# Performance work log

Measured on AMD Instinct MI355X. Metric: run time of the kernel, lower is better.

Reference implementation:

```python
import jax, jax.numpy as jnp
import numpy as np

B, NU, NT = 128, 32, 64          # batch, users/sample, antennas/sample
IN_F, H, OUT_F, NL = 128, 128, 16, 2
N_U, N_A = B * NU, B * NT        # total user / antenna nodes


def setup_inputs() -> dict:
    key = jax.random.key(0)
    ks = iter(jax.random.split(key, 40))
    p = lambda shape: jax.random.normal(next(ks), shape, jnp.float32) * 0.05
    inp = {
        'user_feat': jax.random.normal(next(ks), (N_U, IN_F), jnp.float32),
        'ant_noise': jax.random.normal(next(ks), (N_A, H), jnp.float32),
    }
    # complete bipartite edges within each batch sample
    b = np.arange(B)[:, None, None]
    u = np.arange(NU)[None, :, None]
    t = np.arange(NT)[None, None, :]
    su = np.broadcast_to(b * NU + u, (B, NU, NT)).reshape(-1)  # user global ids
    dt = np.broadcast_to(b * NT + t, (B, NU, NT)).reshape(-1)  # antenna global ids
    inp['src_u2a'] = jnp.asarray(su, jnp.int32)
    inp['dst_u2a'] = jnp.asarray(dt, jnp.int32)
    inp['src_a2u'] = jnp.asarray(dt, jnp.int32)
    inp['dst_a2u'] = jnp.asarray(su, jnp.int32)
    inp['W_ue'] = p((IN_F, H)); inp['b_ue'] = p((H,))
    inp['W_t'] = p((H, H));     inp['b_t'] = p((H,))
    for name in ['ca_aggr', 'ca_self', 'ca_comb', 'cu_aggr', 'cu_self', 'cu_comb']:
        inp[name + '_W'] = p((NL, H, H))
        inp[name + '_b'] = p((NL, H))
    inp['W_norm'] = p((H, OUT_F)); inp['b_norm'] = p((OUT_F,))
    return inp


def mlp(x, W, b):
    # stack of NL Linear(H,H) + ReLU, as in MLP module
    for i in range(W.shape[0]):
        x = jax.nn.relu(x @ W[i] + b[i])
    return x


def rel_conv(src_f, dst_f, src_idx, dst_idx, n_dst, aW, ab, sW, sb, cW, cb):
    # GraphConv2: mean-aggregate mlp_aggr(src) over in-edges, combine with mlp_self(dst)
    msg = mlp(src_f, aW, ab)                                   # [n_src, H]
    summed = jax.ops.segment_sum(msg[src_idx], dst_idx, num_segments=n_dst)
    deg = jax.ops.segment_sum(jnp.ones(dst_idx.shape, jnp.float32), dst_idx,
                              num_segments=n_dst)
    mean = summed / jnp.maximum(deg, 1.0)[:, None]
    return mlp(mlp(dst_f, sW, sb) + mean, cW, cb)


def reference(user_feat, ant_noise, src_u2a, dst_u2a, src_a2u, dst_a2u,
              W_ue, b_ue, W_t, b_t,
              ca_aggr_W, ca_aggr_b, ca_self_W, ca_self_b, ca_comb_W, ca_comb_b,
              cu_aggr_W, cu_aggr_b, cu_self_W, cu_self_b, cu_comb_W, cu_comb_b,
              W_norm, b_norm):
    # InitLayer
    hu = jax.nn.relu(user_feat @ W_ue + b_ue)                  # [B*NU, H]
    ant = jax.nn.relu(hu.reshape(B, NU, H).mean(axis=1) @ W_t + b_t)  # [B, H]
    ha = jnp.repeat(ant, NT, axis=0) + ant_noise               # [B*NT, H]
    # two applications of the SAME HeteroGraphConv (shared weights)
    for _ in range(2):
        na = rel_conv(hu, ha, src_u2a, dst_u2a, N_A,
                      ca_aggr_W, ca_aggr_b, ca_self_W, ca_self_b, ca_comb_W, ca_comb_b)
        nu = rel_conv(ha, hu, src_a2u, dst_a2u, N_U,
                      cu_aggr_W, cu_aggr_b, cu_self_W, cu_self_b, cu_comb_W, cu_comb_b)
        hu, ha = nu, na
    # NormLayer: project, split real/imag, normalize to unit modulus
    y = (ha @ W_norm + b_norm).reshape(B, NT, OUT_F)
    rf = OUT_F // 2
    re, im = y[..., :rf], y[..., rf:]
    mag = jnp.sqrt(re * re + im * im)
    return jnp.concatenate([re / mag, im / mag], axis=-1)      # [B, NT, OUT_F]
```

## Files before the change

### kernel.cpp

```cpp
#include <hip/hip_runtime.h>
#include <math.h>


using frag  = __attribute__((ext_vector_type(8))) short;
using f32x4 = __attribute__((ext_vector_type(4))) float;

#define LDST 136
#define SCOPE_AGT __HIP_MEMORY_SCOPE_AGENT

__device__ __forceinline__ float  bf2f(ushort u) { return __uint_as_float(((unsigned)u) << 16); }
__device__ __forceinline__ ushort f2bf(float f) {
    unsigned u = __float_as_uint(f);
    u += 0x7fff + ((u >> 16) & 1);
    return (ushort)(u >> 16);
}
__device__ __forceinline__ unsigned cvtpk(float lo, float hi) {
    unsigned r;
    asm("v_cvt_pk_bf16_f32 %0, %1, %2" : "=v"(r) : "v"(lo), "v"(hi));
    return r;
}
__device__ __forceinline__ void gst16_sc(void* p, f32x4 v) {
    asm volatile("global_store_dwordx4 %0, %1, off sc1" :: "v"(p), "v"(v) : "memory");
}

struct GP {
    const float *uf, *noise, *b_ue, *W_t, *b_t;
    const float *bias6[6];
    const float *Wn, *bn;
    const ushort *Wp;
    float *out;
    float *pE, *pA0, *pU0, *pA1;
    unsigned *flg;
};

struct PrepP { const float* Wm[13]; ushort* Wp; unsigned* flg; };

__global__ __launch_bounds__(512) void k_prep(PrepP Q)
{
    const int tid = threadIdx.x, blk = blockIdx.x;
    if (blk < 16) Q.flg[blk * 512 + tid] = 0;
    const int e = (blk * 512 + tid) * 8;
    const int l = (e >> 3) & 63, w = (e >> 9) & 7, kc = (e >> 12) & 3, m = e >> 14;
    const float* src = Q.Wm[m] + (kc * 32 + (l >> 4) * 8) * 128 + w * 16 + (l & 15);
    ushort h[8];
#pragma unroll
    for (int j = 0; j < 8; ++j) h[j] = f2bf(src[j * 128]);
    uint4 o = { (unsigned)h[0] | ((unsigned)h[1] << 16), (unsigned)h[2] | ((unsigned)h[3] << 16),
                (unsigned)h[4] | ((unsigned)h[5] << 16), (unsigned)h[6] | ((unsigned)h[7] << 16) };
    *(uint4*)(Q.Wp + e) = o;
}

__device__ __forceinline__ void psync(unsigned* myf, unsigned* pf, unsigned s) {
    asm volatile("s_waitcnt vmcnt(0)" ::: "memory");
    __syncthreads();
    if (threadIdx.x == 0) {
        __hip_atomic_store(myf, s, __ATOMIC_RELAXED, SCOPE_AGT);
        while (__hip_atomic_load(pf, __ATOMIC_RELAXED, SCOPE_AGT) < s)
            __builtin_amdgcn_s_sleep(1);
    }
    __syncthreads();
}

struct AF { frag f[4]; };
__device__ __forceinline__ AF ldA(const ushort* __restrict__ Wp, int mat, int tid)
{
    AF a;
    const ushort* base = Wp + ((size_t)mat << 14) + (tid << 3);
#pragma unroll
    for (int kc = 0; kc < 4; ++kc)
        a.f[kc] = *(const frag*)(base + (kc << 12));
    return a;
}

template<int MT, bool MEANADD, bool CS>
__device__ __forceinline__ void mlp_stage(const AF& A, const ushort* Xl, ushort* Yl,
    const float* biasL, const float* meanL, float* csL, float* __restrict__ csG,
    int n0, int l15, int q)
{
    const float4 bv = *(const float4*)(biasL + n0 + q * 4);
    float4 mv = {0.f, 0.f, 0.f, 0.f};
    if (MEANADD) mv = *(const float4*)(meanL + n0 + q * 4);
    float cs0 = 0.f, cs1 = 0.f, cs2 = 0.f, cs3 = 0.f;
#pragma unroll
    for (int mt = 0; mt < MT; ++mt) {
        frag Bv[4];
#pragma unroll
        for (int kc = 0; kc < 4; ++kc)
            Bv[kc] = *(const frag*)(Xl + (mt * 16 + l15) * LDST + kc * 32 + q * 8);
        f32x4 acc = {0.f, 0.f, 0.f, 0.f};
#pragma unroll
        for (int kc = 0; kc < 4; ++kc)
            acc = __builtin_amdgcn_mfma_f32_16x16x32_bf16(A.f[kc], Bv[kc], acc, 0, 0, 0);
        float v0 = acc[0] + bv.x, v1 = acc[1] + bv.y, v2 = acc[2] + bv.z, v3 = acc[3] + bv.w;
        v0 = v0 > 0.f ? v0 : 0.f; v1 = v1 > 0.f ? v1 : 0.f;
        v2 = v2 > 0.f ? v2 : 0.f; v3 = v3 > 0.f ? v3 : 0.f;
        if (MEANADD) { v0 += mv.x; v1 += mv.y; v2 += mv.z; v3 += mv.w; }
        if (CS) { cs0 += v0; cs1 += v1; cs2 += v2; cs3 += v3; }
        uint2 o = { cvtpk(v0, v1), cvtpk(v2, v3) };
        *(uint2*)(Yl + (mt * 16 + l15) * LDST + n0 + q * 4) = o;
    }
    if (CS) {
#pragma unroll
        for (int m = 1; m <= 8; m <<= 1) {
            cs0 += __shfl_xor(cs0, m); cs1 += __shfl_xor(cs1, m);
            cs2 += __shfl_xor(cs2, m); cs3 += __shfl_xor(cs3, m);
        }
        if (l15 == 0) {
            f32x4 t = { cs0, cs1, cs2, cs3 };
            *(f32x4*)(csL + n0 + q * 4) = t;
            gst16_sc(csG + n0 + q * 4, t);
        }
    }
}

__global__ __launch_bounds__(512, 1) void k_gnn(GP P)
{
    __shared__ __align__(16) ushort HU[16 * LDST];
    __shared__ __align__(16) ushort HA[32 * LDST];
    __shared__ __align__(16) ushort T0[32 * LDST];
    __shared__ __align__(16) ushort T1[32 * LDST];
    __shared__ __align__(16) float  biasL[1792];
    __shared__ __align__(16) float  redL[512];
    __shared__ __align__(16) float  meanP[128], meanQ[128], antL[128];

    const int blk = blockIdx.x, tid = threadIdx.x;
    const int b = blk & 127, half = blk >> 7, prt = blk ^ 128;
    const int lane = tid & 63, wave = tid >> 6;
    const int q = lane >> 4, l15 = lane & 15;
    const int n0 = wave * 16;
    unsigned* myf = P.flg + blk * 32;
    unsigned* prf = P.flg + prt * 32;

    AF An = ldA(P.Wp, 12, tid);

    {
        const int r = tid >> 5, k4 = tid & 31;
        const float4 v = *(const float4*)(P.uf + (size_t)(b * 32 + half * 16 + r) * 128 + k4 * 4);
        uint2 o = { cvtpk(v.x, v.y), cvtpk(v.z, v.w) };
        *(uint2*)(T0 + r * LDST + k4 * 4) = o;
    }
#pragma unroll
    for (int c = tid; c < 1024; c += 512) {
        const int r = c >> 5, k4 = c & 31;
        const float4 v = *(const float4*)(P.noise + (size_t)(b * 64 + half * 32 + r) * 128 + k4 * 4);
        uint2 o = { cvtpk(v.x, v.y), cvtpk(v.z, v.w) };
        *(uint2*)(HA + r * LDST + k4 * 4) = o;
    }
    if (tid < 128) biasL[tid] = P.b_ue[tid];
    if (tid < 128) biasL[1664 + tid] = P.b_t[tid];
#pragma unroll
    for (int r = 0; r < 6; ++r)
        if (tid < 256) biasL[128 + r * 256 + tid] = P.bias6[r][tid];
    __syncthreads();

    AF A;
    A = An; An = ldA(P.Wp, 0, tid);
    mlp_stage<1, false, true>(A, T0, HU, biasL + 0, nullptr, meanP, P.pE + blk * 128, n0, l15, q);
    __syncthreads();
    A = An; An = ldA(P.Wp, 1, tid);
    mlp_stage<1, false, false>(A, HU, T0, biasL + 128, nullptr, nullptr, nullptr, n0, l15, q);
    __syncthreads();
    A = An; An = ldA(P.Wp, 6, tid);
    mlp_stage<1, false, true>(A, T0, T1, biasL + 256, nullptr, meanQ, P.pA0 + blk * 128, n0, l15, q);
    __syncthreads();
    psync(myf, prf, 1u);

    if (tid < 128) {
        meanP[tid] = (meanP[tid] + P.pE[prt * 128 + tid]) * (1.f / 32.f);
        meanQ[tid] = (meanQ[tid] + P.pA0[prt * 128 + tid]) * (1.f / 32.f);
    }
    __syncthreads();
    {
        const int g = tid >> 7, col = tid & 127;
        float s = 0.f;
#pragma unroll 4
        for (int k = g * 32; k < g * 32 + 32; ++k) s += meanP[k] * P.W_t[k * 128 + col];
        redL[g * 128 + col] = s;
    }
    __syncthreads();
    if (tid < 128) {
        float a = biasL[1664 + tid] + redL[tid] + redL[128 + tid] + redL[256 + tid] + redL[384 + tid];
        antL[tid] = a > 0.f ? a : 0.f;
    }
    __syncthreads();
#pragma unroll
    for (int c = tid; c < 1024; c += 512) {
        const int r = c >> 5, k4 = c & 31;
        ushort4 h = *(ushort4*)(HA + r * LDST + k4 * 4);
        uint2 o = { cvtpk(bf2f(h.x) + antL[k4 * 4 + 0], bf2f(h.y) + antL[k4 * 4 + 1]),
                    cvtpk(bf2f(h.z) + antL[k4 * 4 + 2], bf2f(h.w) + antL[k4 * 4 + 3]) };
        *(uint2*)(HA + r * LDST + k4 * 4) = o;
    }
    __syncthreads();

    A = An; An = ldA(P.Wp, 7, tid);
    mlp_stage<2, false, false>(A, HA, T0, biasL + 896, nullptr, nullptr, nullptr, n0, l15, q);
    __syncthreads();
    A = An; An = ldA(P.Wp, 2, tid);
    mlp_stage<2, false, true>(A, T0, T1, biasL + 1024, nullptr, meanP, P.pU0 + blk * 128, n0, l15, q);
    __syncthreads();
    A = An; An = ldA(P.Wp, 3, tid);
    mlp_stage<2, false, false>(A, HA, T0, biasL + 384, nullptr, nullptr, nullptr, n0, l15, q);
    __syncthreads();
    psync(myf, prf, 2u);
    if (tid < 128)
        meanP[tid] = (meanP[tid] + P.pU0[prt * 128 + tid]) * (1.f / 64.f);
    __syncthreads();
    A = An; An = ldA(P.Wp, 4, tid);
    mlp_stage<2, true , false>(A, T0, T1, biasL + 512, meanQ, nullptr, nullptr, n0, l15, q);
    __syncthreads();
    A = An; An = ldA(P.Wp, 5, tid);
    mlp_stage<2, false, false>(A, T1, T0, biasL + 640, nullptr, nullptr, nullptr, n0, l15, q);
    __syncthreads();
    A = An; An = ldA(P.Wp, 8, tid);
    mlp_stage<2, false, false>(A, T0, HA, biasL + 768, nullptr, nullptr, nullptr, n0, l15, q);
    __syncthreads();
    A = An; An = ldA(P.Wp, 9, tid);
    mlp_stage<1, false, false>(A, HU, T0, biasL + 1152, nullptr, nullptr, nullptr, n0, l15, q);
    __syncthreads();
    A = An; An = ldA(P.Wp, 10, tid);
    mlp_stage<1, true , false>(A, T0, T1, biasL + 1280, meanP, nullptr, nullptr, n0, l15, q);
    __syncthreads();
    A = An; An = ldA(P.Wp, 11, tid);
    mlp_stage<1, false, false>(A, T1, T0, biasL + 1408, nullptr, nullptr, nullptr, n0, l15, q);
    __syncthreads();
    A = An; An = ldA(P.Wp, 0, tid);
    mlp_stage<1, false, false>(A, T0, HU, biasL + 1536, nullptr, nullptr, nullptr, n0, l15, q);
    __syncthreads();

    A = An; An = ldA(P.Wp, 1, tid);
    mlp_stage<1, false, false>(A, HU, T0, biasL + 128, nullptr, nullptr, nullptr, n0, l15, q);
    __syncthreads();
    A = An; An = ldA(P.Wp, 2, tid);
    mlp_stage<1, false, true>(A, T0, T1, biasL + 256, nullptr, meanQ, P.pA1 + blk * 128, n0, l15, q);
    __syncthreads();
    A = An; An = ldA(P.Wp, 3, tid);
    mlp_stage<2, false, false>(A, HA, T0, biasL + 384, nullptr, nullptr, nullptr, n0, l15, q);
    __syncthreads();
    psync(myf, prf, 3u);
    if (tid < 128)
        meanQ[tid] = (meanQ[tid] + P.pA1[prt * 128 + tid]) * (1.f / 32.f);
    __syncthreads();
    A = An; An = ldA(P.Wp, 4, tid);
    mlp_stage<2, true , false>(A, T0, T1, biasL + 512, meanQ, nullptr, nullptr, n0, l15, q);
    __syncthreads();
    A = An; An = ldA(P.Wp, 5, tid);
    mlp_stage<2, false, false>(A, T1, T0, biasL + 640, nullptr, nullptr, nullptr, n0, l15, q);
    __syncthreads();
    A = An;
    mlp_stage<2, false, false>(A, T0, T1, biasL + 768, nullptr, nullptr, nullptr, n0, l15, q);
    __syncthreads();

    float* WnS = (float*)T0;
    *(float4*)(WnS + tid * 4) = *(const float4*)(P.Wn + tid * 4);
    __syncthreads();
    {
        const int row = tid >> 4, j = tid & 15;
        float acc = P.bn[j];
        const ushort* h = T1 + row * LDST;
#pragma unroll 8
        for (int k = 0; k < 128; ++k) acc += bf2f(h[k]) * WnS[k * 16 + j];
        const float other = __shfl_xor(acc, 8);
        const float mag = sqrtf(acc * acc + other * other);
        P.out[(size_t)(b * 64 + half * 32 + row) * 16 + j] = acc / mag;
    }
}

extern "C" void kernel_launch(void* const* d_in, const int* in_sizes, int n_in,
                              void* d_out, int out_size, void* d_ws, size_t ws_size,
                              hipStream_t stream)
{
    GP P;
    P.uf    = (const float*)d_in[0];
    P.noise = (const float*)d_in[1];
    const float* W_ue = (const float*)d_in[6];
    P.b_ue  = (const float*)d_in[7];
    P.W_t   = (const float*)d_in[8];
    P.b_t   = (const float*)d_in[9];
    const float* caW[3] = {(const float*)d_in[10], (const float*)d_in[12], (const float*)d_in[14]};
    const float* cab[3] = {(const float*)d_in[11], (const float*)d_in[13], (const float*)d_in[15]};
    const float* cuW[3] = {(const float*)d_in[16], (const float*)d_in[18], (const float*)d_in[20]};
    const float* cub[3] = {(const float*)d_in[17], (const float*)d_in[19], (const float*)d_in[21]};
    P.Wn  = (const float*)d_in[22];
    P.bn  = (const float*)d_in[23];
    P.out = (float*)d_out;

    PrepP Q;
    Q.Wm[0]  = caW[0]; Q.Wm[1]  = caW[0] + 16384;
    Q.Wm[2]  = caW[1]; Q.Wm[3]  = caW[1] + 16384;
    Q.Wm[4]  = caW[2]; Q.Wm[5]  = caW[2] + 16384;
    Q.Wm[6]  = cuW[0]; Q.Wm[7]  = cuW[0] + 16384;
    Q.Wm[8]  = cuW[1]; Q.Wm[9]  = cuW[1] + 16384;
    Q.Wm[10] = cuW[2]; Q.Wm[11] = cuW[2] + 16384;
    Q.Wm[12] = W_ue;
    P.bias6[0] = cab[0]; P.bias6[1] = cab[1]; P.bias6[2] = cab[2];
    P.bias6[3] = cub[0]; P.bias6[4] = cub[1]; P.bias6[5] = cub[2];

    char* w = (char*)d_ws;
    P.flg = (unsigned*)w;
    P.pE  = (float*)(w + 32768);
    P.pA0 = P.pE  + 256 * 128;
    P.pU0 = P.pA0 + 256 * 128;
    P.pA1 = P.pU0 + 256 * 128;
    ushort* Wp = (ushort*)(w + 32768 + 4 * 256 * 128 * 4);
    Q.Wp = Wp;
    Q.flg = P.flg;
    P.Wp = Wp;

    k_prep<<<dim3(52), dim3(512), 0, stream>>>(Q);
    k_gnn<<<dim3(256), dim3(512), 0, stream>>>(P);
}
```

Measured before the change: 121.9 us.

## Merge per-sample block pairs into one 1024-thread block, dropping global flag syncs

Each batch sample is now handled by one 1024-thread block instead of two 512-thread blocks that exchanged partial column sums through global memory and spin-waited on flags. Rows are split across two wave groups, and column sums are combined in shared memory, which removes the cross-block atomics, sleeps and sc1 stores. The final projection loop now reads vectorised uint4 loads. In exchange only 128 blocks run on the GPU, each with twice the LDS footprint, so fewer CUs are occupied and each one has more per-block work.

```diff
diff --git a/kernel.cpp b/kernel.cpp
--- a/kernel.cpp
+++ b/kernel.cpp
@@ -6,7 +6,6 @@
 using f32x4 = __attribute__((ext_vector_type(4))) float;
 
 #define LDST 136
-#define SCOPE_AGT __HIP_MEMORY_SCOPE_AGENT
 
 __device__ __forceinline__ float  bf2f(ushort u) { return __uint_as_float(((unsigned)u) << 16); }
 __device__ __forceinline__ ushort f2bf(float f) {
@@ -18,9 +17,6 @@
     unsigned r;
     asm("v_cvt_pk_bf16_f32 %0, %1, %2" : "=v"(r) : "v"(lo), "v"(hi));
     return r;
-}
-__device__ __forceinline__ void gst16_sc(void* p, f32x4 v) {
-    asm volatile("global_store_dwordx4 %0, %1, off sc1" :: "v"(p), "v"(v) : "memory");
 }
 
 struct GP {
@@ -29,16 +25,13 @@
     const float *Wn, *bn;
     const ushort *Wp;
     float *out;
-    float *pE, *pA0, *pU0, *pA1;
-    unsigned *flg;
 };
 
-struct PrepP { const float* Wm[13]; ushort* Wp; unsigned* flg; };
+struct PrepP { const float* Wm[13]; ushort* Wp; };
 
 __global__ __launch_bounds__(512) void k_prep(PrepP Q)
 {
     const int tid = threadIdx.x, blk = blockIdx.x;
-    if (blk < 16) Q.flg[blk * 512 + tid] = 0;
     const int e = (blk * 512 + tid) * 8;
     const int l = (e >> 3) & 63, w = (e >> 9) & 7, kc = (e >> 12) & 3, m = e >> 14;
     const float* src = Q.Wm[m] + (kc * 32 + (l >> 4) * 8) * 128 + w * 16 + (l & 15);
@@ -50,22 +43,11 @@
     *(uint4*)(Q.Wp + e) = o;
 }
 
-__device__ __forceinline__ void psync(unsigned* myf, unsigned* pf, unsigned s) {
-    asm volatile("s_waitcnt vmcnt(0)" ::: "memory");
-    __syncthreads();
-    if (threadIdx.x == 0) {
-        __hip_atomic_store(myf, s, __ATOMIC_RELAXED, SCOPE_AGT);
-        while (__hip_atomic_load(pf, __ATOMIC_RELAXED, SCOPE_AGT) < s)
-            __builtin_amdgcn_s_sleep(1);
-    }
-    __syncthreads();
-}
-
 struct AF { frag f[4]; };
-__device__ __forceinline__ AF ldA(const ushort* __restrict__ Wp, int mat, int tid)
+__device__ __forceinline__ AF ldA(const ushort* __restrict__ Wp, int mat, int widx)
 {
     AF a;
-    const ushort* base = Wp + ((size_t)mat << 14) + (tid << 3);
+    const ushort* base = Wp + ((size_t)mat << 14) + (widx << 3);
 #pragma unroll
     for (int kc = 0; kc < 4; ++kc)
         a.f[kc] = *(const frag*)(base + (kc << 12));
@@ -74,8 +56,8 @@
 
 template<int MT, bool MEANADD, bool CS>
 __device__ __forceinline__ void mlp_stage(const AF& A, const ushort* Xl, ushort* Yl,
-    const float* biasL, const float* meanL, float* csL, float* __restrict__ csG,
-    int n0, int l15, int q)
+    const float* biasL, const float* meanL, float* csPart,
+    int row0, int n0, int l15, int q)
 {
     const float4 bv = *(const float4*)(biasL + n0 + q * 4);
     float4 mv = {0.f, 0.f, 0.f, 0.f};
@@ -83,10 +65,11 @@
     float cs0 = 0.f, cs1 = 0.f, cs2 = 0.f, cs3 = 0.f;
 #pragma unroll
     for (int mt = 0; mt < MT; ++mt) {
+        const int r = (row0 + mt * 16 + l15) * LDST;
         frag Bv[4];
 #pragma unroll
         for (int kc = 0; kc < 4; ++kc)
-            Bv[kc] = *(const frag*)(Xl + (mt * 16 + l15) * LDST + kc * 32 + q * 8);
+            Bv[kc] = *(const frag*)(Xl + r + kc * 32 + q * 8);
         f32x4 acc = {0.f, 0.f, 0.f, 0.f};
 #pragma unroll
         for (int kc = 0; kc < 4; ++kc)
@@ -97,7 +80,7 @@
         if (MEANADD) { v0 += mv.x; v1 += mv.y; v2 += mv.z; v3 += mv.w; }
         if (CS) { cs0 += v0; cs1 += v1; cs2 += v2; cs3 += v3; }
         uint2 o = { cvtpk(v0, v1), cvtpk(v2, v3) };
-        *(uint2*)(Yl + (mt * 16 + l15) * LDST + n0 + q * 4) = o;
+        *(uint2*)(Yl + r + n0 + q * 4) = o;
     }
     if (CS) {
 #pragma unroll
@@ -107,42 +90,42 @@
         }
         if (l15 == 0) {
             f32x4 t = { cs0, cs1, cs2, cs3 };
-            *(f32x4*)(csL + n0 + q * 4) = t;
-            gst16_sc(csG + n0 + q * 4, t);
+            *(f32x4*)(csPart + n0 + q * 4) = t;
         }
     }
 }
 
-__global__ __launch_bounds__(512, 1) void k_gnn(GP P)
-{
-    __shared__ __align__(16) ushort HU[16 * LDST];
-    __shared__ __align__(16) ushort HA[32 * LDST];
-    __shared__ __align__(16) ushort T0[32 * LDST];
-    __shared__ __align__(16) ushort T1[32 * LDST];
+__global__ __launch_bounds__(1024, 1) void k_gnn(GP P)
+{
+    __shared__ __align__(16) ushort HU[32 * LDST];
+    __shared__ __align__(16) ushort HA[64 * LDST];
+    __shared__ __align__(16) ushort T0[64 * LDST];
+    __shared__ __align__(16) ushort T1[64 * LDST];
     __shared__ __align__(16) float  biasL[1792];
-    __shared__ __align__(16) float  redL[512];
+    __shared__ __align__(16) float  redL[1024];
+    __shared__ __align__(16) float  csL[256];
     __shared__ __align__(16) float  meanP[128], meanQ[128], antL[128];
 
-    const int blk = blockIdx.x, tid = threadIdx.x;
-    const int b = blk & 127, half = blk >> 7, prt = blk ^ 128;
+    const int b = blockIdx.x, tid = threadIdx.x;
     const int lane = tid & 63, wave = tid >> 6;
+    const int wn = wave & 7, wm = wave >> 3;
     const int q = lane >> 4, l15 = lane & 15;
-    const int n0 = wave * 16;
-    unsigned* myf = P.flg + blk * 32;
-    unsigned* prf = P.flg + prt * 32;
-
-    AF An = ldA(P.Wp, 12, tid);
+    const int n0 = wn * 16, widx = wn * 64 + lane;
+    const int huR = wm * 16, haR = wm * 32;
+    float* csP = csL + wm * 128;
+
+    AF An = ldA(P.Wp, 12, widx);
 
     {
         const int r = tid >> 5, k4 = tid & 31;
-        const float4 v = *(const float4*)(P.uf + (size_t)(b * 32 + half * 16 + r) * 128 + k4 * 4);
+        const float4 v = *(const float4*)(P.uf + (size_t)(b * 32 + r) * 128 + k4 * 4);
         uint2 o = { cvtpk(v.x, v.y), cvtpk(v.z, v.w) };
         *(uint2*)(T0 + r * LDST + k4 * 4) = o;
     }
 #pragma unroll
-    for (int c = tid; c < 1024; c += 512) {
+    for (int c = tid; c < 2048; c += 1024) {
         const int r = c >> 5, k4 = c & 31;
-        const float4 v = *(const float4*)(P.noise + (size_t)(b * 64 + half * 32 + r) * 128 + k4 * 4);
+        const float4 v = *(const float4*)(P.noise + (size_t)(b * 64 + r) * 128 + k4 * 4);
         uint2 o = { cvtpk(v.x, v.y), cvtpk(v.z, v.w) };
         *(uint2*)(HA + r * LDST + k4 * 4) = o;
     }
@@ -154,37 +137,34 @@
     __syncthreads();
 
     AF A;
-    A = An; An = ldA(P.Wp, 0, tid);
-    mlp_stage<1, false, true>(A, T0, HU, biasL + 0, nullptr, meanP, P.pE + blk * 128, n0, l15, q);
-    __syncthreads();
-    A = An; An = ldA(P.Wp, 1, tid);
-    mlp_stage<1, false, false>(A, HU, T0, biasL + 128, nullptr, nullptr, nullptr, n0, l15, q);
-    __syncthreads();
-    A = An; An = ldA(P.Wp, 6, tid);
-    mlp_stage<1, false, true>(A, T0, T1, biasL + 256, nullptr, meanQ, P.pA0 + blk * 128, n0, l15, q);
-    __syncthreads();
-    psync(myf, prf, 1u);
-
-    if (tid < 128) {
-        meanP[tid] = (meanP[tid] + P.pE[prt * 128 + tid]) * (1.f / 32.f);
-        meanQ[tid] = (meanQ[tid] + P.pA0[prt * 128 + tid]) * (1.f / 32.f);
-    }
-    __syncthreads();
+    A = An; An = ldA(P.Wp, 0, widx);
+    mlp_stage<1, false, true>(A, T0, HU, biasL + 0, nullptr, csP, huR, n0, l15, q);
+    __syncthreads();
+    if (tid < 128) meanP[tid] = (csL[tid] + csL[128 + tid]) * (1.f / 32.f);
+    A = An; An = ldA(P.Wp, 1, widx);
+    mlp_stage<1, false, false>(A, HU, T0, biasL + 128, nullptr, nullptr, huR, n0, l15, q);
+    __syncthreads();
+    A = An; An = ldA(P.Wp, 6, widx);
+    mlp_stage<1, false, true>(A, T0, T1, biasL + 256, nullptr, csP, huR, n0, l15, q);
+    __syncthreads();
+    if (tid < 128) meanQ[tid] = (csL[tid] + csL[128 + tid]) * (1.f / 32.f);
     {
         const int g = tid >> 7, col = tid & 127;
         float s = 0.f;
 #pragma unroll 4
-        for (int k = g * 32; k < g * 32 + 32; ++k) s += meanP[k] * P.W_t[k * 128 + col];
+        for (int k = g * 16; k < g * 16 + 16; ++k) s += meanP[k] * P.W_t[k * 128 + col];
         redL[g * 128 + col] = s;
     }
     __syncthreads();
     if (tid < 128) {
-        float a = biasL[1664 + tid] + redL[tid] + redL[128 + tid] + redL[256 + tid] + redL[384 + tid];
+        float a = biasL[1664 + tid];
+#pragma unroll
+        for (int i = 0; i < 8; ++i) a += redL[i * 128 + tid];
         antL[tid] = a > 0.f ? a : 0.f;
     }
     __syncthreads();
 #pragma unroll
-    for (int c = tid; c < 1024; c += 512) {
+    for (int c = tid; c < 2048; c += 1024) {
         const int r = c >> 5, k4 = c & 31;
         ushort4 h = *(ushort4*)(HA + r * LDST + k4 * 4);
         uint2 o = { cvtpk(bf2f(h.x) + antL[k4 * 4 + 0], bf2f(h.y) + antL[k4 * 4 + 1]),
@@ -193,76 +173,77 @@
     }
     __syncthreads();
 
-    A = An; An = ldA(P.Wp, 7, tid);
-    mlp_stage<2, false, false>(A, HA, T0, biasL + 896, nullptr, nullptr, nullptr, n0, l15, q);
-    __syncthreads();
-    A = An; An = ldA(P.Wp, 2, tid);
-    mlp_stage<2, false, true>(A, T0, T1, biasL + 1024, nullptr, meanP, P.pU0 + blk * 128, n0, l15, q);
-    __syncthreads();
-    A = An; An = ldA(P.Wp, 3, tid);
-    mlp_stage<2, false, false>(A, HA, T0, biasL + 384, nullptr, nullptr, nullptr, n0, l15, q);
-    __syncthreads();
-    psync(myf, prf, 2u);
-    if (tid < 128)
-        meanP[tid] = (meanP[tid] + P.pU0[prt * 128 + tid]) * (1.f / 64.f);
-    __syncthreads();
-    A = An; An = ldA(P.Wp, 4, tid);
-    mlp_stage<2, true , false>(A, T0, T1, biasL + 512, meanQ, nullptr, nullptr, n0, l15, q);
-    __syncthreads();
-    A = An; An = ldA(P.Wp, 5, tid);
-    mlp_stage<2, false, false>(A, T1, T0, biasL + 640, nullptr, nullptr, nullptr, n0, l15, q);
-    __syncthreads();
-    A = An; An = ldA(P.Wp, 8, tid);
-    mlp_stage<2, false, false>(A, T0, HA, biasL + 768, nullptr, nullptr, nullptr, n0, l15, q);
-    __syncthreads();
-    A = An; An = ldA(P.Wp, 9, tid);
-    mlp_stage<1, false, false>(A, HU, T0, biasL + 1152, nullptr, nullptr, nullptr, n0, l15, q);
-    __syncthreads();
-    A = An; An = ldA(P.Wp, 10, tid);
-    mlp_stage<1, true , false>(A, T0, T1, biasL + 1280, meanP, nullptr, nullptr, n0, l15, q);
-    __syncthreads();
-    A = An; An = ldA(P.Wp, 11, tid);
-    mlp_stage<1, false, false>(A, T1, T0, biasL + 1408, nullptr, nullptr, nullptr, n0, l15, q);
-    __syncthreads();
-    A = An; An = ldA(P.Wp, 0, tid);
-    mlp_stage<1, false, false>(A, T0, HU, biasL + 1536, nullptr, nullptr, nullptr, n0, l15, q);
-    __syncthreads();
-
-    A = An; An = ldA(P.Wp, 1, tid);
-    mlp_stage<1, false, false>(A, HU, T0, biasL + 128, nullptr, nullptr, nullptr, n0, l15, q);
-    __syncthreads();
-    A = An; An = ldA(P.Wp, 2, tid);
-    mlp_stage<1, false, true>(A, T0, T1, biasL + 256, nullptr, meanQ, P.pA1 + blk * 128, n0, l15, q);
-    __syncthreads();
-    A = An; An = ldA(P.Wp, 3, tid);
-    mlp_stage<2, false, false>(A, HA, T0, biasL + 384, nullptr, nullptr, nullptr, n0, l15, q);
-    __syncthreads();
-    psync(myf, prf, 3u);
-    if (tid < 128)
-        meanQ[tid] = (meanQ[tid] + P.pA1[prt * 128 + tid]) * (1.f / 32.f);
-    __syncthreads();
-    A = An; An = ldA(P.Wp, 4, tid);
-    mlp_stage<2, true , false>(A, T0, T1, biasL + 512, meanQ, nullptr, nullptr, n0, l15, q);
-    __syncthreads();
-    A = An; An = ldA(P.Wp, 5, tid);
-    mlp_stage<2, false, false>(A, T1, T0, biasL + 640, nullptr, nullptr, nullptr, n0, l15, q);
+    A = An; An = ldA(P.Wp, 7, widx);
+    mlp_stage<2, false, false>(A, HA, T0, biasL + 896, nullptr, nullptr, haR, n0, l15, q);
+    __syncthreads();
+    A = An; An = ldA(P.Wp, 2, widx);
+    mlp_stage<2, false, true>(A, T0, T1, biasL + 1024, nullptr, csP, haR, n0, l15, q);
+    __syncthreads();
+    if (tid < 128) meanP[tid] = (csL[tid] + csL[128 + tid]) * (1.f / 64.f);
+    A = An; An = ldA(P.Wp, 3, widx);
+    mlp_stage<2, false, false>(A, HA, T0, biasL + 384, nullptr, nullptr, haR, n0, l15, q);
+    __syncthreads();
+    A = An; An = ldA(P.Wp, 4, widx);
+    mlp_stage<2, true , false>(A, T0, T1, biasL + 512, meanQ, nullptr, haR, n0, l15, q);
+    __syncthreads();
+    A = An; An = ldA(P.Wp, 5, widx);
+    mlp_stage<2, false, false>(A, T1, T0, biasL + 640, nullptr, nullptr, haR, n0, l15, q);
+    __syncthreads();
+    A = An; An = ldA(P.Wp, 8, widx);
+    mlp_stage<2, false, false>(A, T0, HA, biasL + 768, nullptr, nullptr, haR, n0, l15, q);
+    __syncthreads();
+    A = An; An = ldA(P.Wp, 9, widx);
+    mlp_stage<1, false, false>(A, HU, T0, biasL + 1152, nullptr, nullptr, huR, n0, l15, q);
+    __syncthreads();
+    A = An; An = ldA(P.Wp, 10, widx);
+    mlp_stage<1, true , false>(A, T0, T1, biasL + 1280, meanP, nullptr, huR, n0, l15, q);
+    __syncthreads();
+    A = An; An = ldA(P.Wp, 11, widx);
+    mlp_stage<1, false, false>(A, T1, T0, biasL + 1408, nullptr, nullptr, huR, n0, l15, q);
+    __syncthreads();
+    A = An; An = ldA(P.Wp, 0, widx);
+    mlp_stage<1, false, false>(A, T0, HU, biasL + 1536, nullptr, nullptr, huR, n0, l15, q);
+    __syncthreads();
+
+    A = An; An = ldA(P.Wp, 1, widx);
+    mlp_stage<1, false, false>(A, HU, T0, biasL + 128, nullptr, nullptr, huR, n0, l15, q);
+    __syncthreads();
+    A = An; An = ldA(P.Wp, 2, widx);
+    mlp_stage<1, false, true>(A, T0, T1, biasL + 256, nullptr, csP, huR, n0, l15, q);
+    __syncthreads();
+    if (tid < 128) meanQ[tid] = (csL[tid] + csL[128 + tid]) * (1.f / 32.f);
+    A = An; An = ldA(P.Wp, 3, widx);
+    mlp_stage<2, false, false>(A, HA, T0, biasL + 384, nullptr, nullptr, haR, n0, l15, q);
+    __syncthreads();
+    A = An; An = ldA(P.Wp, 4, widx);
+    mlp_stage<2, true , false>(A, T0, T1, biasL + 512, meanQ, nullptr, haR, n0, l15, q);
+    __syncthreads();
+    A = An; An = ldA(P.Wp, 5, widx);
+    mlp_stage<2, false, false>(A, T1, T0, biasL + 640, nullptr, nullptr, haR, n0, l15, q);
     __syncthreads();
     A = An;
-    mlp_stage<2, false, false>(A, T0, T1, biasL + 768, nullptr, nullptr, nullptr, n0, l15, q);
+    mlp_stage<2, false, false>(A, T0, T1, biasL + 768, nullptr, nullptr, haR, n0, l15, q);
     __syncthreads();
 
     float* WnS = (float*)T0;
-    *(float4*)(WnS + tid * 4) = *(const float4*)(P.Wn + tid * 4);
+    if (tid < 512) *(float4*)(WnS + tid * 4) = *(const float4*)(P.Wn + tid * 4);
     __syncthreads();
     {
         const int row = tid >> 4, j = tid & 15;
         float acc = P.bn[j];
-        const ushort* h = T1 + row * LDST;
-#pragma unroll 8
-        for (int k = 0; k < 128; ++k) acc += bf2f(h[k]) * WnS[k * 16 + j];
+        const uint4* h4 = (const uint4*)(T1 + row * LDST);
+#pragma unroll
+        for (int kb = 0; kb < 16; ++kb) {
+            const uint4 u = h4[kb];
+            const float* wp = WnS + kb * 128 + j;
+            acc += bf2f((ushort)u.x) * wp[0]   + bf2f((ushort)(u.x >> 16)) * wp[16]
+                 + bf2f((ushort)u.y) * wp[32]  + bf2f((ushort)(u.y >> 16)) * wp[48]
+                 + bf2f((ushort)u.z) * wp[64]  + bf2f((ushort)(u.z >> 16)) * wp[80]
+                 + bf2f((ushort)u.w) * wp[96]  + bf2f((ushort)(u.w >> 16)) * wp[112];
+        }
         const float other = __shfl_xor(acc, 8);
         const float mag = sqrtf(acc * acc + other * other);
-        P.out[(size_t)(b * 64 + half * 32 + row) * 16 + j] = acc / mag;
+        P.out[(size_t)(b * 64 + row) * 16 + j] = acc / mag;
     }
 }
 
@@ -296,17 +277,10 @@
     P.bias6[0] = cab[0]; P.bias6[1] = cab[1]; P.bias6[2] = cab[2];
     P.bias6[3] = cub[0]; P.bias6[4] = cub[1]; P.bias6[5] = cub[2];
 
-    char* w = (char*)d_ws;
-    P.flg = (unsigned*)w;
-    P.pE  = (float*)(w + 32768);
-    P.pA0 = P.pE  + 256 * 128;
-    P.pU0 = P.pA0 + 256 * 128;
-    P.pA1 = P.pU0 + 256 * 128;
-    ushort* Wp = (ushort*)(w + 32768 + 4 * 256 * 128 * 4);
+    ushort* Wp = (ushort*)d_ws;
     Q.Wp = Wp;
-    Q.flg = P.flg;
     P.Wp = Wp;
 
     k_prep<<<dim3(52), dim3(512), 0, stream>>>(Q);
-    k_gnn<<<dim3(256), dim3(512), 0, stream>>>(P);
-}
+    k_gnn<<<dim3(128), dim3(1024), 0, stream>>>(P);
+}
```

New measurement: 123.8 us. No clear change (+1.6%).
